# Kernel tuning notes

Measured on AMD Instinct MI355X. Metric: run time of the kernel, lower is better.

Reference implementation:

```python
import jax, jax.numpy as jnp
import numpy as np

L2_IDX = np.array([0, 1, 2, 4, 24, 26, 35, 38])
S = 16    # n_scalar_features
H = 32    # hidden multiplicity
NL2 = 9   # number of 2e inputs (8 selected kernels + kernel sum)
B = 131072
NK = 40   # n_kernels


def _w3j_222():
    """Wigner 3j / CG tensor for 2e x 2e -> 2e in the real spherical-harmonic
    basis, Frobenius-normalized (e3nn convention up to an overall sign).
    Computed as the 1-D null space of the infinitesimal equivariance constraint."""
    l = 2
    mv = np.arange(-l, l + 1)
    Jp = np.zeros((5, 5), complex)
    for i, m in enumerate(mv[:-1]):
        Jp[i + 1, i] = np.sqrt(l * (l + 1) - m * (m + 1))
    Jm = Jp.conj().T
    Jx, Jy, Jz = (Jp + Jm) / 2, (Jp - Jm) / 2j, np.diag(mv).astype(complex)
    # complex -> real spherical harmonics change of basis
    Q = np.zeros((5, 5), complex)
    for m in mv:
        i = m + l
        if m < 0:
            Q[i, i] = 1j / np.sqrt(2)
            Q[i, l - m] = -1j * (-1.0) ** m / np.sqrt(2)
        elif m == 0:
            Q[i, i] = 1.0
        else:
            Q[i, l - m] = 1 / np.sqrt(2)
            Q[i, i] = (-1.0) ** m / np.sqrt(2)
    Gs = [np.real(-1j * Q @ J @ Q.conj().T) for J in (Jx, Jy, Jz)]  # real so(3) generators
    I5, I25 = np.eye(5), np.eye(25)
    M = np.concatenate([np.kron(G, I25) + np.kron(I5, np.kron(G, I5)) + np.kron(I25, G)
                        for G in Gs], axis=0)
    c = np.linalg.svd(M)[2][-1].reshape(5, 5, 5)
    c = c / np.linalg.norm(c)
    if c.flat[np.argmax(np.abs(c))] < 0:
        c = -c
    return c.astype(np.float32)


C222 = jnp.asarray(_w3j_222())
INV_SQRT5 = float(1.0 / np.sqrt(5.0))  # CG value for l,l->0 and 0,l->l paths


def setup_inputs() -> dict:
    key = jax.random.key(0)
    ks = jax.random.split(key, 10)
    return {
        "scalars": jax.random.normal(ks[0], (B, S), jnp.float32),
        "kernel_t2s": jax.random.normal(ks[1], (B, NK, 5), jnp.float32),
        "w000": jax.random.normal(ks[2], (S, S, H), jnp.float32),
        "w110": jax.random.normal(ks[3], (NL2, NL2, H), jnp.float32),
        "w011": jax.random.normal(ks[4], (S, NL2, H), jnp.float32),
        "w101": jax.random.normal(ks[5], (NL2, S, H), jnp.float32),
        "w111": jax.random.normal(ks[6], (NL2, NL2, H), jnp.float32),
        "v010": jax.random.normal(ks[7], (H, H), jnp.float32),
        "v100": jax.random.normal(ks[8], (H, H), jnp.float32),
        "v110": jax.random.normal(ks[9], (H, H), jnp.float32),
    }


def reference(scalars, kernel_t2s, w000, w110, w011, w101, w111, v010, v100, v110):
    s = scalars                                                  # (B, S)   0e inputs
    t = jnp.concatenate([kernel_t2s[:, L2_IDX, :],
                         kernel_t2s.sum(axis=1, keepdims=True)], axis=1)  # (B, 9, 5) 2e inputs

    # e3nn path-normalization coefficients (component / element defaults)
    c0 = (1.0 / (S * S + NL2 * NL2 * 5)) ** 0.5   # 0e out: fan-in S*S + 9*9*... -> S^2 + 81
    c0 = (1.0 / (S * S + 81)) ** 0.5
    c2 = (5.0 / (18 * S + 81)) ** 0.5             # 2e out: fan-in 9S + 9S + 81

    # ---- tp1(x, x): hidden = Hx0e + Hx2e ----
    h0 = c0 * (jnp.einsum('uvw,bu,bv->bw', w000, s, s)
               + INV_SQRT5 * jnp.einsum('uvw,bui,bvi->bw', w110, t, t))          # (B, H)
    u1 = jnp.einsum('bui,ijk->bujk', t, C222)                                    # (B,9,5,5)
    u2 = jnp.einsum('bujk,bvj->buvk', u1, t)                                     # (B,9,9,5)
    h2 = c2 * (INV_SQRT5 * jnp.einsum('uvw,bu,bvk->bwk', w011, s, t)
               + INV_SQRT5 * jnp.einsum('uvw,bui,bv->bwi', w101, t, s)
               + jnp.einsum('buvk,uvw->bwk', u2, w111))                          # (B, H, 5)

    # ---- tp2(h, h): 1x2e ----
    d = (5.0 / (3 * H * H)) ** 0.5
    a = jnp.einsum('uv,bvj->buj', v110, h2)       # (B, H, 5)
    b2 = jnp.einsum('bui,buj->bij', h2, a)        # (B, 5, 5)
    out = d * (INV_SQRT5 * (jnp.einsum('uv,bu,bvk->bk', v010, h0, h2)
                            + jnp.einsum('uv,buk,bv->bk', v100, h2, h0))
               + jnp.einsum('bij,ijk->bk', b2, C222))                            # (B, 5)
    return out
```

## Files before the change

### kernel.cpp

```cpp
#include <hip/hip_runtime.h>
#include <cmath>


#define DEVINL static __device__ __forceinline__

typedef _Float16 half2_t __attribute__((ext_vector_type(2)));
typedef _Float16 half8_t __attribute__((ext_vector_type(8)));
typedef float    f32x4_t __attribute__((ext_vector_type(4)));
union H8 { half8_t v; half2_t p[4]; };

#define FW0   0
#define FWC   6144
#define FMR   15360
#define HW111 16384
#define HV110 18176
#define SLABH 19456

__device__ __align__(16) _Float16 g_wsh[SLABH];

struct CPack { float v[32]; };

static constexpr int CIa[32] = {2,2,2,4,2,4,4,4, 2,0,0, 2,1,1, 2,3,3, 4,0,0, 4,1,1, 4,3,3, 0,0,1,1,3,3};
static constexpr int CJa[32] = {2,2,4,2,4,2,4,4, 0,2,0, 1,2,1, 3,2,3, 0,4,0, 1,4,1, 3,4,3, 1,3,0,3,0,1};
static constexpr int CKa[32] = {2,4,2,2,4,4,2,4, 0,0,2, 1,1,2, 3,3,2, 0,0,4, 1,1,4, 3,3,4, 3,1,3,0,1,0};

__host__ __device__ inline void tri_uv(int p, int n, int& u, int& v) {
  int base = 0;
  for (int x = 0; x < n; x++) {
    int c = n - x;
    if (p < base + c) { u = x; v = x + (p - base); return; }
    base += c;
  }
  u = n - 1; v = n - 1;
}

static double h_trE3(const double A[3][3], const double B[3][3], const double C[3][3]) {
  double t = 0.0;
  for (int r = 0; r < 3; r++)
    for (int c = 0; c < 3; c++) {
      double ab = 0.0;
      for (int m = 0; m < 3; m++) ab += A[r][m] * B[m][c];
      t += ab * C[c][r];
    }
  return t;
}
static void computeC(CPack& out) {
  const double s2i = 0.7071067811865475244, s6i = 0.4082482904638630164;
  double E[5][3][3] = {
    {{0, s2i, 0}, {s2i, 0, 0}, {0, 0, 0}},
    {{0, 0, 0}, {0, 0, s2i}, {0, s2i, 0}},
    {{-s6i, 0, 0}, {0, -s6i, 0}, {0, 0, 2.0 * s6i}},
    {{0, 0, s2i}, {0, 0, 0}, {s2i, 0, 0}},
    {{s2i, 0, 0}, {0, -s2i, 0}, {0, 0, 0}}
  };
  double T[125], nrm = 0.0;
  for (int f = 0; f < 125; f++) {
    int i = f / 25, j = (f / 5) % 5, k = f % 5;
    T[f] = h_trE3(E[i], E[j], E[k]) + h_trE3(E[i], E[k], E[j]);
    nrm += T[f] * T[f];
  }
  nrm = std::sqrt(nrm);
  int am = 0; double mx = std::fabs(T[0]);
  for (int q = 1; q < 125; q++) { double v = std::fabs(T[q]); if (v > mx) { mx = v; am = q; } }
  const double scale = ((T[am] < 0.0) ? 1.0 : -1.0) / nrm;
  for (int s = 0; s < 32; s++)
    out.v[s] = (float)(scale * T[(CIa[s] * 5 + CJa[s]) * 5 + CKa[s]]);
}

DEVINL float dot2f(half2_t a, half2_t b, float c) {
#if __has_builtin(__builtin_amdgcn_fdot2)
  return __builtin_amdgcn_fdot2(a, b, c, false);
#else
  return fmaf((float)a[0], (float)b[0], fmaf((float)a[1], (float)b[1], c));
#endif
}
DEVINL half2_t pk2(float a, float b) {
  auto r = __builtin_amdgcn_cvt_pkrtz(a, b);
  half2_t o;
  __builtin_memcpy(&o, &r, sizeof(o));
  return o;
}
DEVINL int h2i(half2_t h) { int i; __builtin_memcpy(&i, &h, 4); return i; }
DEVINL half2_t i2h(int i) { half2_t h; __builtin_memcpy(&h, &i, 4); return h; }
DEVINL f32x4_t mfma16(half8_t a, half8_t b, f32x4_t c) {
  return __builtin_amdgcn_mfma_f32_16x16x32_f16(a, b, c, 0, 0, 0);
}
DEVINL void store4h(_Float16* p, f32x4_t d) {
  int2 v;
  v.x = h2i(pk2(d[0], d[1]));
  v.y = h2i(pk2(d[2], d[3]));
  *(int2*)p = v;
}

__global__ void ech_setup(const float* __restrict__ w000, const float* __restrict__ w110,
                          const float* __restrict__ w011, const float* __restrict__ w101,
                          const float* __restrict__ w111, const float* __restrict__ v010,
                          const float* __restrict__ v100, const float* __restrict__ v110) {
  const float c0   = 1.0f / sqrtf(337.0f);
  const float inv5 = 0.44721359549995794f;
  const float c2   = sqrtf(5.0f / 369.0f);
  const float dm   = sqrtf(5.0f / 3072.0f) * inv5;
  int gid = blockIdx.x * blockDim.x + threadIdx.x;
  int gs  = gridDim.x * blockDim.x;

  for (int idx = gid; idx < 6144; idx += gs) {
    int j = idx & 7, L = (idx >> 3) & 63, tk = idx >> 9;
    int mt = tk / 6, ks = tk % 6;
    int w = mt * 16 + (L & 15);
    int p = ks * 32 + (L >> 4) * 8 + j;
    float x = 0.0f;
    if (p < 136) {
      int u, v; tri_uv(p, 16, u, v);
      x = c0 * (w000[(u * 16 + v) * 32 + w] + (u != v ? w000[(v * 16 + u) * 32 + w] : 0.0f));
    } else if (p < 181) {
      int u, v; tri_uv(p - 136, 9, u, v);
      x = c0 * inv5 * (w110[(u * 9 + v) * 32 + w] + (u != v ? w110[(v * 9 + u) * 32 + w] : 0.0f));
    }
    g_wsh[FW0 + idx] = (_Float16)x;
  }
  for (int idx = gid; idx < 9216; idx += gs) {
    int j = idx & 7, L = (idx >> 3) & 63, t = idx >> 9;
    int m = t * 16 + (L & 15);
    int w = m / 9, v = m % 9;
    int u = (L >> 4) * 8 + j;
    float x = (u < 16) ? c2 * inv5 * (w011[(u * 9 + v) * 32 + w] + w101[(v * 16 + u) * 32 + w]) : 0.0f;
    g_wsh[FWC + idx] = (_Float16)x;
  }
  for (int idx = gid; idx < 1024; idx += gs) {
    int j = idx & 7, L = (idx >> 3) & 63, mt = idx >> 9;
    int w = mt * 16 + (L & 15);
    int u = (L >> 4) * 8 + j;
    g_wsh[FMR + idx] = (_Float16)(dm * (v010[u * 32 + w] + v100[w * 32 + u]));
  }
  for (int idx = gid; idx < 32 * 56; idx += gs) {
    int w = idx / 56, p = idx % 56; float x = 0.0f;
    if (p < 45) { int u, v; tri_uv(p, 9, u, v);
      x = c2 * (w111[(u * 9 + v) * 32 + w] + (u != v ? w111[(v * 9 + u) * 32 + w] : 0.0f)); }
    g_wsh[HW111 + w * 56 + p] = (_Float16)x;
  }
  for (int idx = gid; idx < 1024; idx += gs) {
    int u = idx / 32, v = idx % 32;
    g_wsh[HV110 + u * 40 + v] = (_Float16)v110[u * 32 + v];
  }
}

#define ESZ 440
__global__ void __launch_bounds__(512)
ech_main(const float* __restrict__ sc, const float* __restrict__ t2s,
         float* __restrict__ out, int nGroups, CPack C) {
  __shared__ __align__(16) _Float16 slabh[SLABH];
  __shared__ __align__(16) float scr[16 * ESZ];
  __shared__ __align__(16) _Float16 cvvH[16 * 296];
  __shared__ __align__(16) _Float16 h0st[16 * 40];
  __shared__ __align__(16) _Float16 gst[16 * 40];
  __shared__ int pairs9[48];
  __shared__ int sspair[68];

  const int tid  = threadIdx.x;
  const int lane = tid & 31;
  const int sub  = tid >> 5;
  const int w    = lane;

  for (int i = tid; i < SLABH / 8; i += 512)
    ((float4*)slabh)[i] = ((const float4*)g_wsh)[i];
  if (tid < 45) { int u, v; tri_uv(tid, 9, u, v); pairs9[tid] = u | (v << 4); }
  if (tid < 68) {
    int u0, v0, u1, v1;
    tri_uv(2 * tid, 16, u0, v0);
    tri_uv(2 * tid + 1, 16, u1, v1);
    sspair[tid] = u0 | (v0 << 4) | (u1 << 8) | (v1 << 12);
  }
  __syncthreads();

  constexpr int L2R[8] = {0, 1, 2, 4, 24, 26, 35, 38};

  float*     E    = scr + sub * ESZ;
  float*     Araw = E;
  _Float16*  qhh  = (_Float16*)E;
  _Float16*  h2hh = (_Float16*)(E + 120);
  float*     tb   = E + 200;
  _Float16*  sshh = (_Float16*)(E + 272);
  _Float16*  tthh = (_Float16*)(E + 340);
  _Float16*  thh  = (_Float16*)(E + 368);
  float*     sL   = E + 408;
  int*       spad = (int*)(E + 424);

  for (int grp = blockIdx.x; grp < nGroups; grp += gridDim.x) {
    const int b = grp * 16 + sub;

    {
      const float4* src = (const float4*)(t2s + (size_t)b * 200);
      float4* Av = (float4*)Araw;
      Av[lane] = src[lane];
      if (lane < 18) Av[lane + 32] = src[lane + 32];
    }
    {
      const float4* sv = (const float4*)(sc + (size_t)b * 16);
      if (lane < 4) ((float4*)sL)[lane] = sv[lane];
    }
    if (lane < 16)
      spad[lane] = (lane < 8) ? h2i(pk2(sL[2 * lane], sL[2 * lane + 1])) : 0;

    #pragma unroll
    for (int it = 0; it < 2; it++) {
      int idx = lane + 32 * it;
      if (idx < 40) {
        int r = idx / 5, c = idx % 5;
        float val = Araw[L2R[r] * 5 + c];
        tb[r * 8 + c] = val;
        thh[c * 16 + r] = (_Float16)val;
      }
    }
    {
      int l25 = lane % 25;
      int c2 = l25 / 5, j2 = l25 % 5;
      float acc = 0.f;
      #pragma unroll
      for (int rr = 0; rr < 8; rr++) acc += Araw[(j2 + 5 * rr) * 5 + c2];
      float tot = __shfl(acc, 5 * c2 + 0, 32) + __shfl(acc, 5 * c2 + 1, 32)
                + __shfl(acc, 5 * c2 + 2, 32) + __shfl(acc, 5 * c2 + 3, 32)
                + __shfl(acc, 5 * c2 + 4, 32);
      if (lane < 25 && j2 == 0) { tb[64 + c2] = tot; thh[c2 * 16 + 8] = (_Float16)tot; }
    }
    if (lane < 31) {
      if (lane < 15)      qhh[(lane / 3) * 48 + 45 + lane % 3] = (_Float16)0.f;
      else if (lane < 26) tthh[45 + (lane - 15)] = (_Float16)0.f;
      else                thh[(lane - 26) * 16 + 9] = (_Float16)0.f;
    }

    #pragma unroll
    for (int it = 0; it < 2; it++) {
      int idx = lane + 32 * it;
      if (idx < 45) {
        int pr = pairs9[idx];
        int pu = pr & 15, pv = pr >> 4;
        float4 u4 = *(const float4*)(tb + pu * 8); float u5 = tb[pu * 8 + 4];
        float4 v4 = *(const float4*)(tb + pv * 8); float v5 = tb[pv * 8 + 4];
        float tu[5] = {u4.x, u4.y, u4.z, u4.w, u5};
        float tv[5] = {v4.x, v4.y, v4.z, v4.w, v5};
        float tt = tu[0]*tv[0] + tu[1]*tv[1] + tu[2]*tv[2] + tu[3]*tv[3] + tu[4]*tv[4];
        tthh[idx] = (_Float16)tt;
        float qk[5] = {0, 0, 0, 0, 0};
        #pragma unroll
        for (int s = 0; s < 32; s++)
          qk[CKa[s]] = fmaf(C.v[s], tu[CIa[s]] * tv[CJa[s]], qk[CKa[s]]);
        #pragma unroll
        for (int k = 0; k < 5; k++) qhh[k * 48 + idx] = (_Float16)qk[k];
      }
    }

    #pragma unroll
    for (int ii = 0; ii < 3; ii++) {
      int slot = lane + 32 * ii;
      if (slot < 68) {
        int t = sspair[slot];
        int u0 = t & 15, v0 = (t >> 4) & 15, u1 = (t >> 8) & 15, v1 = (t >> 12) & 15;
        *(half2_t*)(sshh + 2 * slot) = pk2(sL[u0] * sL[v0], sL[u1] * sL[v1]);
      }
    }
    __syncthreads();

    {
      const int wid = tid >> 6;
      const int L   = tid & 63;
      const int e2  = L & 15;
      const int q2  = L >> 4;
      const _Float16* scrH = (const _Float16*)scr;
      if (wid == 0) {
        f32x4_t a0 = {0.f, 0.f, 0.f, 0.f}, a1 = {0.f, 0.f, 0.f, 0.f};
        const _Float16* ssb = scrH + e2 * 880 + 544;
        #pragma unroll
        for (int ks = 0; ks < 6; ks++) {
          half8_t bb = *(const half8_t*)(ssb + ks * 32 + q2 * 8);
          half8_t w0 = *(const half8_t*)(slabh + FW0 + ks * 512 + L * 8);
          half8_t w1 = *(const half8_t*)(slabh + FW0 + (6 + ks) * 512 + L * 8);
          a0 = mfma16(w0, bb, a0);
          a1 = mfma16(w1, bb, a1);
        }
        store4h(h0st + e2 * 40 + q2 * 4, a0);
        store4h(h0st + e2 * 40 + 16 + q2 * 4, a1);
        half8_t hb = *(const half8_t*)(h0st + e2 * 40 + q2 * 8);
        half8_t m0 = *(const half8_t*)(slabh + FMR + L * 8);
        half8_t m1 = *(const half8_t*)(slabh + FMR + 512 + L * 8);
        f32x4_t z4 = {0.f, 0.f, 0.f, 0.f};
        f32x4_t g0 = mfma16(m0, hb, z4);
        f32x4_t g1 = mfma16(m1, hb, z4);
        store4h(gst + e2 * 40 + q2 * 4, g0);
        store4h(gst + e2 * 40 + 16 + q2 * 4, g1);
      } else if (wid <= 2) {
        const _Float16* spb = scrH + e2 * 880 + 848;
        half8_t bb = *(const half8_t*)(spb + q2 * 8);
        const int t0 = (wid - 1) * 9;
        #pragma unroll
        for (int t = 0; t < 9; t++) {
          half8_t wa = *(const half8_t*)(slabh + FWC + (t0 + t) * 512 + L * 8);
          f32x4_t z4 = {0.f, 0.f, 0.f, 0.f};
          f32x4_t d = mfma16(wa, bb, z4);
          store4h(cvvH + e2 * 296 + (t0 + t) * 16 + q2 * 4, d);
        }
      }
    }
    __syncthreads();

    float Cvv[9];
    #pragma unroll
    for (int v = 0; v < 9; v++) Cvv[v] = (float)cvvH[sub * 296 + w * 9 + v];
    half2_t cpk[5] = { pk2(Cvv[0], Cvv[1]), pk2(Cvv[2], Cvv[3]),
                       pk2(Cvv[4], Cvv[5]), pk2(Cvv[6], Cvv[7]), pk2(Cvv[8], 0.f) };
    float h2r[5];
    #pragma unroll
    for (int k = 0; k < 5; k++) {
      H8 d; d.v = *(const half8_t*)(thh + k * 16);
      half2_t d4 = *(const half2_t*)(thh + k * 16 + 8);
      float acc = dot2f(cpk[0], d.p[0], 0.f);
      acc = dot2f(cpk[1], d.p[1], acc);
      acc = dot2f(cpk[2], d.p[2], acc);
      acc = dot2f(cpk[3], d.p[3], acc);
      acc = dot2f(cpk[4], d4, acc);
      h2r[k] = acc;
    }

    {
      H8 wk[6];
      const _Float16* wr = slabh + HW111 + w * 56;
      #pragma unroll
      for (int i = 0; i < 6; i++) wk[i].v = *(const half8_t*)(wr + 8 * i);
      #pragma unroll
      for (int k = 0; k < 5; k++) {
        const _Float16* qr = qhh + k * 48;
        float accA = h2r[k], accB = 0.f;
        #pragma unroll
        for (int i = 0; i < 6; i++) {
          H8 d; d.v = *(const half8_t*)(qr + 8 * i);
          accA = dot2f(wk[i].p[0], d.p[0], accA); accB = dot2f(wk[i].p[1], d.p[1], accB);
          accA = dot2f(wk[i].p[2], d.p[2], accA); accB = dot2f(wk[i].p[3], d.p[3], accB);
        }
        h2r[k] = accA + accB;
      }
    }

    #pragma unroll
    for (int k = 0; k < 5; k++) h2hh[k * 32 + w] = (_Float16)h2r[k];

    float a5[5];
    {
      H8 wk[4];
      const _Float16* wr = slabh + HV110 + w * 40;
      #pragma unroll
      for (int i = 0; i < 4; i++) wk[i].v = *(const half8_t*)(wr + 8 * i);
      #pragma unroll
      for (int j = 0; j < 5; j++) {
        const _Float16* hr = h2hh + j * 32;
        float accA = 0.f, accB = 0.f;
        #pragma unroll
        for (int i = 0; i < 4; i++) {
          H8 d; d.v = *(const half8_t*)(hr + 8 * i);
          accA = dot2f(wk[i].p[0], d.p[0], accA); accB = dot2f(wk[i].p[1], d.p[1], accB);
          accA = dot2f(wk[i].p[2], d.p[2], accA); accB = dot2f(wk[i].p[3], d.p[3], accB);
        }
        a5[j] = accA + accB;
      }
    }

    float g = (float)gst[sub * 40 + w];

    float yv[5] = {0, 0, 0, 0, 0};
    #pragma unroll
    for (int s = 0; s < 32; s++)
      yv[CKa[s]] = fmaf(C.v[s], h2r[CIa[s]] * a5[CJa[s]], yv[CKa[s]]);

    const float DCONST = sqrtf(5.0f / 3072.0f);
    float z[5];
    #pragma unroll
    for (int k = 0; k < 5; k++) z[k] = fmaf(DCONST, yv[k], g * h2r[k]);

    half2_t z01 = pk2(z[0], z[1]);
    half2_t z23 = pk2(z[2], z[3]);
    float   z4r = z[4];
    #pragma unroll
    for (int st = 1; st <= 16; st <<= 1) {
      z01 = z01 + i2h(__shfl_xor(h2i(z01), st));
      z23 = z23 + i2h(__shfl_xor(h2i(z23), st));
      z4r += __shfl_xor(z4r, st);
    }
    if (lane < 5) {
      float val = (lane == 0) ? (float)z01[0]
                : (lane == 1) ? (float)z01[1]
                : (lane == 2) ? (float)z23[0]
                : (lane == 3) ? (float)z23[1] : z4r;
      out[(size_t)b * 5 + lane] = val;
    }
  }
}

extern "C" void kernel_launch(void* const* d_in, const int* in_sizes, int n_in,
                              void* d_out, int out_size, void* d_ws, size_t ws_size,
                              hipStream_t stream) {
  (void)n_in; (void)out_size; (void)d_ws; (void)ws_size;

  CPack C;
  computeC(C);

  ech_setup<<<64, 256, 0, stream>>>(
      (const float*)d_in[2], (const float*)d_in[3], (const float*)d_in[4],
      (const float*)d_in[5], (const float*)d_in[6], (const float*)d_in[7],
      (const float*)d_in[8], (const float*)d_in[9]);

  const int B = in_sizes[0] / 16;
  const int nGroups = B / 16;
  ech_main<<<512, 512, 0, stream>>>(
      (const float*)d_in[0], (const float*)d_in[1], (float*)d_out, nGroups, C);
}
```

Before: 261.8 us.

## Move w111 and v110 contractions from per-lane dot2 loops onto MFMA

```diff
diff --git a/kernel.cpp b/kernel.cpp
--- a/kernel.cpp
+++ b/kernel.cpp
@@ -11,10 +11,10 @@
 
 #define FW0   0
 #define FWC   6144
-#define FMR   15360
-#define HW111 16384
-#define HV110 18176
-#define SLABH 19456
+#define FMR   10752
+#define FW111 11776
+#define FV110 13824
+#define SLABH 14848
 
 __device__ __align__(16) _Float16 g_wsh[SLABH];
 
@@ -118,13 +118,13 @@
     }
     g_wsh[FW0 + idx] = (_Float16)x;
   }
-  for (int idx = gid; idx < 9216; idx += gs) {
-    int j = idx & 7, L = (idx >> 3) & 63, t = idx >> 9;
+  for (int idx = gid; idx < 4608; idx += gs) {
+    int j = idx & 7, L = (idx >> 3) & 31, t = idx >> 8;
     int m = t * 16 + (L & 15);
     int w = m / 9, v = m % 9;
     int u = (L >> 4) * 8 + j;
-    float x = (u < 16) ? c2 * inv5 * (w011[(u * 9 + v) * 32 + w] + w101[(v * 16 + u) * 32 + w]) : 0.0f;
-    g_wsh[FWC + idx] = (_Float16)x;
+    g_wsh[FWC + idx] =
+        (_Float16)(c2 * inv5 * (w011[(u * 9 + v) * 32 + w] + w101[(v * 16 + u) * 32 + w]));
   }
   for (int idx = gid; idx < 1024; idx += gs) {
     int j = idx & 7, L = (idx >> 3) & 63, mt = idx >> 9;
@@ -132,25 +132,34 @@
     int u = (L >> 4) * 8 + j;
     g_wsh[FMR + idx] = (_Float16)(dm * (v010[u * 32 + w] + v100[w * 32 + u]));
   }
-  for (int idx = gid; idx < 32 * 56; idx += gs) {
-    int w = idx / 56, p = idx % 56; float x = 0.0f;
+  for (int idx = gid; idx < 2048; idx += gs) {
+    int j = idx & 7, L = (idx >> 3) & 63, t = idx >> 9;
+    int mt = t >> 1, ks = t & 1;
+    int w = mt * 16 + (L & 15);
+    int p = ks * 32 + (L >> 4) * 8 + j;
+    float x = 0.0f;
     if (p < 45) { int u, v; tri_uv(p, 9, u, v);
       x = c2 * (w111[(u * 9 + v) * 32 + w] + (u != v ? w111[(v * 9 + u) * 32 + w] : 0.0f)); }
-    g_wsh[HW111 + w * 56 + p] = (_Float16)x;
+    g_wsh[FW111 + idx] = (_Float16)x;
   }
   for (int idx = gid; idx < 1024; idx += gs) {
-    int u = idx / 32, v = idx % 32;
-    g_wsh[HV110 + u * 40 + v] = (_Float16)v110[u * 32 + v];
-  }
-}
-
-#define ESZ 440
+    int j = idx & 7, L = (idx >> 3) & 63, mt = idx >> 9;
+    int u = mt * 16 + (L & 15);
+    int v = (L >> 4) * 8 + j;
+    g_wsh[FV110 + idx] = (_Float16)v110[u * 32 + v];
+  }
+}
+
+#define ESZ 444
+#define P5MT 272
+#define P5K  544
 __global__ void __launch_bounds__(512)
 ech_main(const float* __restrict__ sc, const float* __restrict__ t2s,
          float* __restrict__ out, int nGroups, CPack C) {
   __shared__ __align__(16) _Float16 slabh[SLABH];
   __shared__ __align__(16) float scr[16 * ESZ];
-  __shared__ __align__(16) _Float16 cvvH[16 * 296];
+  __shared__ __align__(16) _Float16 unionH[5280];
+  __shared__ __align__(16) _Float16 cvvH[16 * 288];
   __shared__ __align__(16) _Float16 h0st[16 * 40];
   __shared__ __align__(16) _Float16 gst[16 * 40];
   __shared__ int pairs9[48];
@@ -160,6 +169,9 @@
   const int lane = tid & 31;
   const int sub  = tid >> 5;
   const int w    = lane;
+
+  _Float16* p5H  = unionH;
+  _Float16* h2Bb = unionH + 2720;
 
   for (int i = tid; i < SLABH / 8; i += 512)
     ((float4*)slabh)[i] = ((const float4*)g_wsh)[i];
@@ -170,14 +182,12 @@
     tri_uv(2 * tid + 1, 16, u1, v1);
     sspair[tid] = u0 | (v0 << 4) | (u1 << 8) | (v1 << 12);
   }
-  __syncthreads();
 
   constexpr int L2R[8] = {0, 1, 2, 4, 24, 26, 35, 38};
 
   float*     E    = scr + sub * ESZ;
   float*     Araw = E;
-  _Float16*  qhh  = (_Float16*)E;
-  _Float16*  h2hh = (_Float16*)(E + 120);
+  _Float16*  qBe  = (_Float16*)E;
   float*     tb   = E + 200;
   _Float16*  sshh = (_Float16*)(E + 272);
   _Float16*  tthh = (_Float16*)(E + 340);
@@ -185,6 +195,11 @@
   float*     sL   = E + 408;
   int*       spad = (int*)(E + 424);
 
+  if (lane < 11)      tthh[45 + lane] = (_Float16)0.f;
+  else if (lane < 16) thh[(lane - 11) * 16 + 9] = (_Float16)0.f;
+  if (lane >= 24)     spad[lane - 16] = 0;
+  __syncthreads();
+
   for (int grp = blockIdx.x; grp < nGroups; grp += gridDim.x) {
     const int b = grp * 16 + sub;
 
@@ -193,13 +208,10 @@
       float4* Av = (float4*)Araw;
       Av[lane] = src[lane];
       if (lane < 18) Av[lane + 32] = src[lane + 32];
-    }
-    {
       const float4* sv = (const float4*)(sc + (size_t)b * 16);
       if (lane < 4) ((float4*)sL)[lane] = sv[lane];
     }
-    if (lane < 16)
-      spad[lane] = (lane < 8) ? h2i(pk2(sL[2 * lane], sL[2 * lane + 1])) : 0;
+    if (lane < 8) spad[lane] = h2i(pk2(sL[2 * lane], sL[2 * lane + 1]));
 
     #pragma unroll
     for (int it = 0; it < 2; it++) {
@@ -221,11 +233,6 @@
                 + __shfl(acc, 5 * c2 + 2, 32) + __shfl(acc, 5 * c2 + 3, 32)
                 + __shfl(acc, 5 * c2 + 4, 32);
       if (lane < 25 && j2 == 0) { tb[64 + c2] = tot; thh[c2 * 16 + 8] = (_Float16)tot; }
-    }
-    if (lane < 31) {
-      if (lane < 15)      qhh[(lane / 3) * 48 + 45 + lane % 3] = (_Float16)0.f;
-      else if (lane < 26) tthh[45 + (lane - 15)] = (_Float16)0.f;
-      else                thh[(lane - 26) * 16 + 9] = (_Float16)0.f;
     }
 
     #pragma unroll
@@ -245,7 +252,10 @@
         for (int s = 0; s < 32; s++)
           qk[CKa[s]] = fmaf(C.v[s], tu[CIa[s]] * tv[CJa[s]], qk[CKa[s]]);
         #pragma unroll
-        for (int k = 0; k < 5; k++) qhh[k * 48 + idx] = (_Float16)qk[k];
+        for (int k = 0; k < 5; k++) qBe[k * 64 + idx] = (_Float16)qk[k];
+      } else {
+        #pragma unroll
+        for (int k = 0; k < 5; k++) qBe[k * 64 + idx] = (_Float16)0.f;
       }
     }
 
@@ -268,43 +278,52 @@
       const _Float16* scrH = (const _Float16*)scr;
       if (wid == 0) {
         f32x4_t a0 = {0.f, 0.f, 0.f, 0.f}, a1 = {0.f, 0.f, 0.f, 0.f};
-        const _Float16* ssb = scrH + e2 * 880 + 544;
+        const _Float16* ssb = scrH + e2 * (2 * ESZ) + 544;
         #pragma unroll
         for (int ks = 0; ks < 6; ks++) {
           half8_t bb = *(const half8_t*)(ssb + ks * 32 + q2 * 8);
-          half8_t w0 = *(const half8_t*)(slabh + FW0 + ks * 512 + L * 8);
-          half8_t w1 = *(const half8_t*)(slabh + FW0 + (6 + ks) * 512 + L * 8);
-          a0 = mfma16(w0, bb, a0);
-          a1 = mfma16(w1, bb, a1);
+          a0 = mfma16(*(const half8_t*)(slabh + FW0 + ks * 512 + L * 8), bb, a0);
+          a1 = mfma16(*(const half8_t*)(slabh + FW0 + (6 + ks) * 512 + L * 8), bb, a1);
         }
         store4h(h0st + e2 * 40 + q2 * 4, a0);
         store4h(h0st + e2 * 40 + 16 + q2 * 4, a1);
         half8_t hb = *(const half8_t*)(h0st + e2 * 40 + q2 * 8);
-        half8_t m0 = *(const half8_t*)(slabh + FMR + L * 8);
-        half8_t m1 = *(const half8_t*)(slabh + FMR + 512 + L * 8);
         f32x4_t z4 = {0.f, 0.f, 0.f, 0.f};
-        f32x4_t g0 = mfma16(m0, hb, z4);
-        f32x4_t g1 = mfma16(m1, hb, z4);
+        f32x4_t g0 = mfma16(*(const half8_t*)(slabh + FMR + L * 8), hb, z4);
+        f32x4_t g1 = mfma16(*(const half8_t*)(slabh + FMR + 512 + L * 8), hb, z4);
         store4h(gst + e2 * 40 + q2 * 4, g0);
         store4h(gst + e2 * 40 + 16 + q2 * 4, g1);
       } else if (wid <= 2) {
-        const _Float16* spb = scrH + e2 * 880 + 848;
+        const _Float16* spb = scrH + e2 * (2 * ESZ) + 848;
         half8_t bb = *(const half8_t*)(spb + q2 * 8);
         const int t0 = (wid - 1) * 9;
+        half8_t wz = {0, 0, 0, 0, 0, 0, 0, 0};
         #pragma unroll
         for (int t = 0; t < 9; t++) {
-          half8_t wa = *(const half8_t*)(slabh + FWC + (t0 + t) * 512 + L * 8);
+          half8_t wa = (q2 < 2) ? *(const half8_t*)(slabh + FWC + (t0 + t) * 256 + L * 8) : wz;
           f32x4_t z4 = {0.f, 0.f, 0.f, 0.f};
           f32x4_t d = mfma16(wa, bb, z4);
-          store4h(cvvH + e2 * 296 + (t0 + t) * 16 + q2 * 4, d);
+          store4h(cvvH + e2 * 288 + (t0 + t) * 16 + q2 * 4, d);
         }
+      } else {
+        const int k = wid - 3;
+        const _Float16* qb = scrH + e2 * (2 * ESZ) + k * 64;
+        f32x4_t d0 = {0.f, 0.f, 0.f, 0.f}, d1 = {0.f, 0.f, 0.f, 0.f};
+        #pragma unroll
+        for (int ks = 0; ks < 2; ks++) {
+          half8_t bb = *(const half8_t*)(qb + ks * 32 + q2 * 8);
+          d0 = mfma16(*(const half8_t*)(slabh + FW111 + ks * 512 + L * 8), bb, d0);
+          d1 = mfma16(*(const half8_t*)(slabh + FW111 + (2 + ks) * 512 + L * 8), bb, d1);
+        }
+        store4h(p5H + k * P5K + e2 * 16 + q2 * 4, d0);
+        store4h(p5H + k * P5K + P5MT + e2 * 16 + q2 * 4, d1);
       }
     }
     __syncthreads();
 
     float Cvv[9];
     #pragma unroll
-    for (int v = 0; v < 9; v++) Cvv[v] = (float)cvvH[sub * 296 + w * 9 + v];
+    for (int v = 0; v < 9; v++) Cvv[v] = (float)cvvH[sub * 288 + w * 9 + v];
     half2_t cpk[5] = { pk2(Cvv[0], Cvv[1]), pk2(Cvv[2], Cvv[3]),
                        pk2(Cvv[4], Cvv[5]), pk2(Cvv[6], Cvv[7]), pk2(Cvv[8], 0.f) };
     float h2r[5];
@@ -317,51 +336,33 @@
       acc = dot2f(cpk[2], d.p[2], acc);
       acc = dot2f(cpk[3], d.p[3], acc);
       acc = dot2f(cpk[4], d4, acc);
-      h2r[k] = acc;
-    }
+      h2r[k] = acc + (float)p5H[k * P5K + (w >> 4) * P5MT + sub * 16 + (w & 15)];
+    }
+    #pragma unroll
+    for (int k = 0; k < 5; k++) h2Bb[k * 512 + sub * 32 + w] = (_Float16)h2r[k];
+    __syncthreads();
 
     {
-      H8 wk[6];
-      const _Float16* wr = slabh + HW111 + w * 56;
-      #pragma unroll
-      for (int i = 0; i < 6; i++) wk[i].v = *(const half8_t*)(wr + 8 * i);
-      #pragma unroll
-      for (int k = 0; k < 5; k++) {
-        const _Float16* qr = qhh + k * 48;
-        float accA = h2r[k], accB = 0.f;
-        #pragma unroll
-        for (int i = 0; i < 6; i++) {
-          H8 d; d.v = *(const half8_t*)(qr + 8 * i);
-          accA = dot2f(wk[i].p[0], d.p[0], accA); accB = dot2f(wk[i].p[1], d.p[1], accB);
-          accA = dot2f(wk[i].p[2], d.p[2], accA); accB = dot2f(wk[i].p[3], d.p[3], accB);
-        }
-        h2r[k] = accA + accB;
+      const int wid = tid >> 6;
+      const int L   = tid & 63;
+      const int e2  = L & 15;
+      const int q2  = L >> 4;
+      if (wid < 5) {
+        const int j = wid;
+        half8_t bb = *(const half8_t*)(h2Bb + j * 512 + e2 * 32 + q2 * 8);
+        f32x4_t z4 = {0.f, 0.f, 0.f, 0.f};
+        f32x4_t d0 = mfma16(*(const half8_t*)(slabh + FV110 + L * 8), bb, z4);
+        f32x4_t d1 = mfma16(*(const half8_t*)(slabh + FV110 + 512 + L * 8), bb, z4);
+        store4h(p5H + j * P5K + e2 * 16 + q2 * 4, d0);
+        store4h(p5H + j * P5K + P5MT + e2 * 16 + q2 * 4, d1);
       }
     }
-
-    #pragma unroll
-    for (int k = 0; k < 5; k++) h2hh[k * 32 + w] = (_Float16)h2r[k];
+    __syncthreads();
 
     float a5[5];
-    {
-      H8 wk[4];
-      const _Float16* wr = slabh + HV110 + w * 40;
-      #pragma unroll
-      for (int i = 0; i < 4; i++) wk[i].v = *(const half8_t*)(wr + 8 * i);
-      #pragma unroll
-      for (int j = 0; j < 5; j++) {
-        const _Float16* hr = h2hh + j * 32;
-        float accA = 0.f, accB = 0.f;
-        #pragma unroll
-        for (int i = 0; i < 4; i++) {
-          H8 d; d.v = *(const half8_t*)(hr + 8 * i);
-          accA = dot2f(wk[i].p[0], d.p[0], accA); accB = dot2f(wk[i].p[1], d.p[1], accB);
-          accA = dot2f(wk[i].p[2], d.p[2], accA); accB = dot2f(wk[i].p[3], d.p[3], accB);
-        }
-        a5[j] = accA + accB;
-      }
-    }
-
+    #pragma unroll
+    for (int j = 0; j < 5; j++)
+      a5[j] = (float)p5H[j * P5K + (w >> 4) * P5MT + sub * 16 + (w & 15)];
     float g = (float)gst[sub * 40 + w];
 
     float yv[5] = {0, 0, 0, 0, 0};
```

New measurement: 251.4 us. 4.0% less time.
